# Performance work log

Measured on AMD Instinct MI355X. Metric: run time of the kernel, lower is better.

The kernel has to match this reference:

```python
import jax, jax.numpy as jnp
import numpy as np
from jax import lax

NUM_ITER = 10
SMOOTH = 1.0
CL_WEIGHT = 0.5


def _min_pool(x, wh, ww):
    # torch: -max_pool2d(-x) pads with -inf -> min-pool with +inf boundary
    return lax.reduce_window(x, jnp.inf, lax.min,
                             (1, 1, wh, ww), (1, 1, 1, 1),
                             [(0, 0), (0, 0), (wh // 2, wh // 2), (ww // 2, ww // 2)])


def _max_pool(x, wh, ww):
    return lax.reduce_window(x, -jnp.inf, lax.max,
                             (1, 1, wh, ww), (1, 1, 1, 1),
                             [(0, 0), (0, 0), (wh // 2, wh // 2), (ww // 2, ww // 2)])


def soft_erode(img):
    return jnp.minimum(_min_pool(img, 3, 1), _min_pool(img, 1, 3))


def soft_dilate(img):
    return _max_pool(img, 3, 3)


def soft_open(img):
    return soft_dilate(soft_erode(img))


def soft_skeleton(img, num_iter=NUM_ITER):
    # img: (B,1,H,W)
    skel = jax.nn.relu(img - soft_open(img))

    def body(i, carry):
        img_e, skel = carry
        img_e = soft_erode(img_e)
        delta = jax.nn.relu(img_e - soft_open(img_e))
        skel = skel + jax.nn.relu(delta - skel * delta)
        return (img_e, skel)

    _, skel = lax.fori_loop(0, num_iter, body, (img, skel))
    return skel


def soft_dice(pred, target, smooth=SMOOTH):
    inter = jnp.sum(pred * target)
    return (2.0 * inter + smooth) / (jnp.sum(pred) + jnp.sum(target) + smooth)


def setup_inputs() -> dict:
    key = jax.random.key(0)
    k1, k2 = jax.random.split(key)
    pred = jax.random.normal(k1, (8, 1, 1024, 1024), dtype=jnp.float32)
    target = jax.random.randint(k2, (8, 1, 1024, 1024), 0, 2, dtype=jnp.int32)
    return {"pred": pred, "target": target}


def reference(pred, target):
    pred_prob = jax.nn.sigmoid(pred)          # (B,1,H,W)
    target_f = target.astype(pred_prob.dtype)

    skel_pred = soft_skeleton(pred_prob)
    skel_target = soft_skeleton(target_f)

    tprec = (jnp.sum(skel_pred * target_f) + SMOOTH) / (jnp.sum(skel_pred) + SMOOTH)
    tsens = (jnp.sum(skel_target * pred_prob) + SMOOTH) / (jnp.sum(skel_target) + SMOOTH)
    cl_dice = 2.0 * tprec * tsens / (tprec + tsens + 1e-7)

    dice = soft_dice(pred_prob, target_f)
    combined = (1.0 - CL_WEIGHT) * dice + CL_WEIGHT * cl_dice
    loss = 1.0 - combined
    return loss
```

## Files before the change

kernel.cpp:

```cpp
#include <hip/hip_runtime.h>
#include <math.h>

#define IMG  1024
#define TILE 64
#define HALO 12
#define SPP  52
#define NPRED (90*SPP)
#define SEN2 0x40004000u

typedef _Float16 h2 __attribute__((ext_vector_type(2)));
union UH { unsigned u; h2 h; };
__device__ __forceinline__ h2 u2h(unsigned u){ UH x; x.u=u; return x.h; }
__device__ __forceinline__ unsigned h2u(h2 h){ UH x; x.h=h; return x.u; }
__device__ __forceinline__ h2 pmin(h2 a, h2 b){ return __builtin_elementwise_min(a,b); }
__device__ __forceinline__ h2 pmax(h2 a, h2 b){ return __builtin_elementwise_max(a,b); }
__device__ __forceinline__ h2 funnel(h2 hi_src, h2 lo_src){
  return u2h((h2u(lo_src)>>16) | (h2u(hi_src)<<16));
}
__device__ __forceinline__ unsigned dpp_shr1(unsigned old_, unsigned src){
  return (unsigned)__builtin_amdgcn_update_dpp((int)old_, (int)src, 0x111, 0xF, 0xF, false);
}
__device__ __forceinline__ unsigned dpp_shl1(unsigned old_, unsigned src){
  return (unsigned)__builtin_amdgcn_update_dpp((int)old_, (int)src, 0x101, 0xF, 0xF, false);
}
__device__ __forceinline__ float sigmoidf(float x){ return 1.0f/(1.0f+__expf(-x)); }
__device__ __forceinline__ h2 unsent(h2 x, h2 onev, h2 zerov){
  h2 t = pmax(x-onev, zerov); return x - t - t;
}
__device__ __forceinline__ unsigned extract8(unsigned w0, unsigned w1, unsigned w2, int bp){
  unsigned long long lo = (unsigned long long)w0 | ((unsigned long long)w1<<32);
  unsigned long long hi = (unsigned long long)w1 | ((unsigned long long)w2<<32);
  unsigned a = (unsigned)(lo >> bp);
  unsigned b = (unsigned)(hi >> (bp & 31));
  return ((bp < 32) ? a : b) & 0xFFu;
}
__device__ __forceinline__ uint4 erode5(uint4 rm, uint4 rc, uint4 rn, h2 lw, h2 rv){
  h2 a0=u2h(rc.x), a1=u2h(rc.y), a2=u2h(rc.z), a3=u2h(rc.w);
  h2 v0=pmin(u2h(rm.x), u2h(rn.x));
  h2 v1=pmin(u2h(rm.y), u2h(rn.y));
  h2 v2=pmin(u2h(rm.z), u2h(rn.z));
  h2 v3=pmin(u2h(rm.w), u2h(rn.w));
  h2 f0=funnel(a0,lw), f1=funnel(a1,a0), f2=funnel(a2,a1), f3=funnel(a3,a2), f4=funnel(rv,a3);
  uint4 e;
  e.x=h2u(pmin(pmin(f0,f1),pmin(v0,a0)));
  e.y=h2u(pmin(pmin(f1,f2),pmin(v1,a1)));
  e.z=h2u(pmin(pmin(f2,f3),pmin(v2,a2)));
  e.w=h2u(pmin(pmin(f3,f4),pmin(v3,a3)));
  return e;
}

template<bool BND>
__device__ void pipeline(const float* __restrict__ pred, const int* __restrict__ targ,
                         long base, int gr0, int gc0, int tid,
                         unsigned* A, unsigned* B, unsigned* Ta, unsigned* Tb,
                         h2 val[4], h2 skel[4], unsigned &tbits, unsigned &skbits) {
  for (int i = tid; i < 104; i += 512) {
    int r = (i < 52) ? 0 : 89, c = (i < 52) ? i : i - 52;
    A[r*SPP + c] = SEN2;  B[r*SPP + c] = SEN2;
  }
  for (int i = tid; i < 704; i += 512) {
    int r = 1 + (i >> 3), w = i & 7;
    w = (w < 2) ? w : 44 + w;
    A[r*SPP + w] = SEN2;  B[r*SPP + w] = SEN2;
  }
  if (!BND) {
    #pragma unroll
    for (int k=0;k<2;++k){
      int u = tid + (k<<9);
      if (u < 968){
        int r = u/11, q = u - r*11;
        long g = base + (long)(gr0+r)*IMG + gc0 + (q<<3);
        float4 pa = *(const float4*)(pred+g);
        float4 pb = *(const float4*)(pred+g+4);
        h2 w0 = {(_Float16)sigmoidf(pa.x), (_Float16)sigmoidf(pa.y)};
        h2 w1 = {(_Float16)sigmoidf(pa.z), (_Float16)sigmoidf(pa.w)};
        h2 w2 = {(_Float16)sigmoidf(pb.x), (_Float16)sigmoidf(pb.y)};
        h2 w3 = {(_Float16)sigmoidf(pb.z), (_Float16)sigmoidf(pb.w)};
        int o = (1+r)*SPP + 2 + (q<<2);
        uint2 d0; d0.x=h2u(w0); d0.y=h2u(w1);
        uint2 d1; d1.x=h2u(w2); d1.y=h2u(w3);
        *(uint2*)&A[o]   = d0;
        *(uint2*)&A[o+2] = d1;
      }
    }
    if (tid < 264){
      int u = tid;
      int r = u/3, w = u - r*3;
      long g = base + (long)(gr0+r)*IMG + gc0 + (w<<5);
      unsigned bits = 0;
      #pragma unroll
      for (int i=0;i<8;++i){
        if (w < 2 || i < 6) {
          int4 tv = *(const int4*)(targ + g + (i<<2));
          unsigned nib = (unsigned)(tv.x!=0) | ((unsigned)(tv.y!=0)<<1)
                       | ((unsigned)(tv.z!=0)<<2) | ((unsigned)(tv.w!=0)<<3);
          bits |= nib << (i<<2);
        }
      }
      if (w==2) bits |= 0xFF000000u;
      Ta[u] = bits;
    }
  } else {
    for (int i=tid; i<88*44; i+=512){
      int r = i/44, wd = i - r*44;
      int gr = gr0 + r;
      bool rok = (unsigned)gr < (unsigned)IMG;
      int gca = gc0 + (wd<<1), gcb = gca + 1;
      _Float16 va = (_Float16)2.0f, vb = (_Float16)2.0f;
      if (rok && (unsigned)gca < (unsigned)IMG) va = (_Float16)sigmoidf(pred[base + (long)gr*IMG + gca]);
      if (rok && (unsigned)gcb < (unsigned)IMG) vb = (_Float16)sigmoidf(pred[base + (long)gr*IMG + gcb]);
      h2 w; w.x = va; w.y = vb;
      A[(1+r)*SPP + 2 + wd] = h2u(w);
    }
    for (int u=tid; u<264; u+=512){
      int r = u/3, w = u - r*3;
      int gr = gr0 + r;
      bool rok = (unsigned)gr < (unsigned)IMG;
      unsigned bits = 0;
      for (int b=0;b<32;++b){
        int c = (w<<5) + b;
        unsigned bit = 1;
        if (c < 88) {
          int gc = gc0 + c;
          if (rok && (unsigned)gc < (unsigned)IMG) bit = (unsigned)(targ[base+(long)gr*IMG+gc] != 0);
        }
        bits |= bit << b;
      }
      Ta[u] = bits;
    }
  }
  __syncthreads();

  unsigned cm0=~0u, cm1=~0u, cm2=0x00FFFFFFu;
  bool colO = false;
  if (BND) {
    int lo = (-gc0 > 0) ? -gc0 : 0;
    int hi = (IMG - gc0 < 88) ? (IMG - gc0) : 88;
    colO = (lo > 0) || (hi < 88);
    unsigned m[3];
    #pragma unroll
    for (int w=0; w<3; ++w){
      int l = lo - (w<<5); if (l<0) l=0;
      int h = hi - (w<<5); if (h>32) h=32;
      unsigned mm = 0;
      if (h > l) {
        unsigned top = (h>=32)? ~0u : ((1u<<h)-1u);
        unsigned bot = (l<=0)? 0u : ((1u<<l)-1u);
        mm = top & ~bot;
      }
      m[w]=mm;
    }
    cm0=m[0]; cm1=m[1]; cm2=m[2] & 0x00FFFFFF;
  }

  const int es  = tid / 12,  eq  = tid - es*12;
  const int s2  = es*2;
  const int ew  = eq << 2;
  const bool has2 = (tid < 16);
  const int u2  = 512 + tid;
  const int es2 = u2/12, eq2 = u2 - es2*12;
  const int s2b = es2*2, ew2 = eq2<<2;

  const bool tex = (tid < 258);
  const int  to  = 3 + tid;
  const int  twd = tid % 3;

  const int qc = tid & 7;
  const int rg = tid >> 3;
  const int pr = HALO + rg;
  const int wq = 8 + (qc<<2);
  const int bp = 12 + (qc<<3);

  h2 ep[4];
  {
    uint4 a0 = *(const uint4*)&A[(pr+1)*SPP + wq];
    ep[0]=u2h(a0.x); ep[1]=u2h(a0.y); ep[2]=u2h(a0.z); ep[3]=u2h(a0.w);
    #pragma unroll
    for (int i=0;i<4;++i){ val[i]=ep[i]; skel[i]=(h2)(_Float16)0.0f; }
  }
  {
    int oa = pr*3;
    tbits = extract8(Ta[oa],Ta[oa+1],Ta[oa+2],bp);
  }
  unsigned tp0=0,tp1=0,tp2=0, sk0=0,sk1=0,sk2=0;
  const bool td = (tid < 64);
  const int tro = (12 + tid)*3;
  if (td) { tp0=Ta[tro]; tp1=Ta[tro+1]; tp2=Ta[tro+2]; }

  const h2 onev  = {(_Float16)1.0f,(_Float16)1.0f};
  const h2 zerov = {(_Float16)0.0f,(_Float16)0.0f};

  for (int j=0;j<11;++j){
    {
      auto ERO = [&](int s2_, int ew_, int eq_){
        uint4 rm = *(const uint4*)&A[s2_*SPP + ew_];
        uint4 rc = *(const uint4*)&A[(s2_+1)*SPP + ew_];
        #pragma unroll
        for (int t=0;t<2;++t){
          uint4 rn = *(const uint4*)&A[(s2_+2+t)*SPP + ew_];
          int brc = s2_+1+t;
          unsigned lwu = SEN2, rvu = SEN2;
          if (((tid&15)==0)  && (eq_!=0))  lwu = A[brc*SPP + ew_ - 1];
          if (((tid&15)==15) && (eq_!=11)) rvu = A[brc*SPP + ew_ + 4];
          lwu = dpp_shr1(lwu, rc.w);
          rvu = dpp_shl1(rvu, rc.x);
          if (eq_==0)  lwu = SEN2;
          if (eq_==11) rvu = SEN2;
          *(uint4*)&B[brc*SPP + ew_] = erode5(rm, rc, rn, u2h(lwu), u2h(rvu));
          rm = rc; rc = rn;
        }
      };
      if ((s2+1 >= j+1) && (s2 <= 86-j))
        ERO(s2, ew, eq);
      if (has2 && (s2b+1 >= j+1) && (s2b <= 86-j))
        ERO(s2b, ew2, eq2);
    }
    if (tex){
      unsigned own=Ta[to], up=Ta[to-3], dn=Ta[to+3];
      unsigned lef=0, rif=0;
      if (((tid&15)==0)  && (twd>0)) lef = Ta[to-1];
      if (((tid&15)==15) && (twd<2)) rif = Ta[to+1];
      unsigned le = dpp_shr1(lef, own);
      unsigned ri = dpp_shl1(rif, own);
      if (twd==0) le = ~0u;
      if (twd==2) ri = ~0u;
      unsigned h = own & ((own>>1)|(ri<<31)) & ((own<<1)|(le>>31));
      Tb[to] = h & up & dn;
    }
    __syncthreads();

    if (BND) {
      if (gr0 < 0) {
        for (int i=tid;i<12*44;i+=512){ int r=i/44; B[(1+r)*SPP+2+(i-r*44)] = SEN2; }
        if (tid < 36) Tb[tid] = ~0u;
      }
      if (gr0 + 88 > IMG) {
        for (int i=tid;i<12*44;i+=512){ int r=i/44; B[(77+r)*SPP+2+(i-r*44)] = SEN2; }
        if (tid < 36) Tb[228+tid] = ~0u;
      }
      if (colO) {
        if (gc0 < 0)
          for (int i=tid;i<88*6;i+=512){ int r=i/6; B[(1+r)*SPP+2+(i-r*6)] = SEN2; }
        if (gc0 + 88 > IMG)
          for (int i=tid;i<88*6;i+=512){ int r=i/6; B[(1+r)*SPP+40+(i-r*6)] = SEN2; }
        for (int i=tid;i<264;i+=512){
          int r=i/3, w=i-r*3;
          unsigned nm = (w==0)?~cm0:((w==1)?~cm1:~cm2);
          Tb[i] |= nm;
        }
      }
      __syncthreads();
    }

    {
      h2 vm[4];
      uint4 cap;
      #pragma unroll
      for (int k=0;k<3;++k){
        int ro = (pr+k)*SPP + wq;
        uint4 c = *(const uint4*)&B[ro];
        unsigned lwu = dpp_shr1(0u, c.w);
        unsigned rwu = dpp_shl1(0u, c.x);
        if (qc==0) lwu = B[ro-1];
        if (qc==7) rwu = B[ro+4];
        if (k==1) cap = c;
        h2 a0=u2h(c.x),a1=u2h(c.y),a2=u2h(c.z),a3=u2h(c.w);
        h2 lwv=u2h(lwu), rwv=u2h(rwu);
        if (BND){
          a0=unsent(a0,onev,zerov); a1=unsent(a1,onev,zerov);
          a2=unsent(a2,onev,zerov); a3=unsent(a3,onev,zerov);
          lwv=unsent(lwv,onev,zerov); rwv=unsent(rwv,onev,zerov);
        }
        h2 f0=funnel(a0,lwv), f1=funnel(a1,a0), f2=funnel(a2,a1), f3=funnel(a3,a2), f4=funnel(rwv,a3);
        h2 h0=pmax(pmax(f0,f1),a0);
        h2 h1=pmax(pmax(f1,f2),a1);
        h2 h2v=pmax(pmax(f2,f3),a2);
        h2 h3=pmax(pmax(f3,f4),a3);
        if (k==0){ vm[0]=h0; vm[1]=h1; vm[2]=h2v; vm[3]=h3; }
        else     { vm[0]=pmax(vm[0],h0); vm[1]=pmax(vm[1],h1);
                   vm[2]=pmax(vm[2],h2v); vm[3]=pmax(vm[3],h3); }
      }
      #pragma unroll
      for (int i=0;i<4;++i){
        h2 d0 = pmax(ep[i]-vm[i], zerov);
        h2 x0 = d0 - skel[i]*d0;
        skel[i] = skel[i] + pmax(x0, zerov);
      }
      ep[0]=u2h(cap.x); ep[1]=u2h(cap.y); ep[2]=u2h(cap.z); ep[3]=u2h(cap.w);
    }

    if (td) {
      unsigned o0=Tb[tro], o1=Tb[tro+1], o2=Tb[tro+2];
      unsigned u0=Tb[tro-3], u1=Tb[tro-2], u2v=Tb[tro-1];
      unsigned n0=Tb[tro+3], n1=Tb[tro+4], n2=Tb[tro+5];
      unsigned v0,v1,v2;
      if (BND){
        unsigned mu = ((unsigned)(gr0 + 11 + tid) < (unsigned)IMG) ? ~0u : 0u;
        unsigned md = ((unsigned)(gr0 + 13 + tid) < (unsigned)IMG) ? ~0u : 0u;
        v0 = ((u0&mu)|o0|(n0&md)) & cm0;
        v1 = ((u1&mu)|o1|(n1&md)) & cm1;
        v2 = ((u2v&mu)|o2|(n2&md)) & cm2;
      } else {
        v0 = u0|o0|n0; v1 = u1|o1|n1; v2 = u2v|o2|n2;
      }
      unsigned d0 = v0 | (v0<<1) | (v0>>1) | (v1<<31);
      unsigned d1 = v1 | (v1<<1) | (v0>>31) | (v1>>1) | (v2<<31);
      unsigned d2 = v2 | (v2<<1) | (v1>>31) | (v2>>1);
      sk0 |= tp0 & ~d0;
      sk1 |= tp1 & ~d1;
      sk2 |= tp2 & ~d2;
      tp0 = o0; tp1 = o1; tp2 = o2;
    }
    unsigned* t1 = A;  A = B;  B = t1;
    unsigned* t2 = Ta; Ta = Tb; Tb = t2;
  }

  __syncthreads();
  if (td){ Ta[3*tid]=sk0; Ta[3*tid+1]=sk1; Ta[3*tid+2]=sk2; }
  __syncthreads();
  {
    int o = rg*3;
    skbits = extract8(Ta[o],Ta[o+1],Ta[o+2],bp);
  }
}

__global__ __launch_bounds__(512,4)
void cl_dice_main(const float* __restrict__ pred, const int* __restrict__ targ,
                  float* __restrict__ ws) {
  __shared__ alignas(16) unsigned sPA[NPRED];
  __shared__ alignas(16) unsigned sPB[NPRED];
  __shared__ unsigned sTA[264], sTB[264];
  const int tid = threadIdx.x;
  const int gr0 = blockIdx.y * TILE - HALO;
  const int gc0 = blockIdx.x * TILE - HALO;
  const long base = (long)blockIdx.z * (long)(IMG * IMG);

  h2 val[4], skel[4]; unsigned tbits, skbits;
  const bool bnd = (blockIdx.x == 0) | (blockIdx.x == gridDim.x - 1) |
                   (blockIdx.y == 0) | (blockIdx.y == gridDim.y - 1);
  if (!bnd) pipeline<false>(pred, targ, base, gr0, gc0, tid, sPA, sPB, sTA, sTB, val, skel, tbits, skbits);
  else      pipeline<true >(pred, targ, base, gr0, gc0, tid, sPA, sPB, sTA, sTB, val, skel, tbits, skbits);

  float s[7] = {0,0,0,0,0,0,0};
  #pragma unroll
  for (int k=0;k<4;++k){
    int bb = k<<1;
    float p0=(float)val[k].x,  p1=(float)val[k].y;
    float a0=(float)skel[k].x, a1=(float)skel[k].y;
    float t0=(float)((tbits>>bb)&1u),  t1=(float)((tbits>>(bb+1))&1u);
    float b0=(float)((skbits>>bb)&1u), b1=(float)((skbits>>(bb+1))&1u);
    s[0]+=a0+a1;        s[1]+=a0*t0+a1*t1;
    s[2]+=b0+b1;        s[3]+=b0*p0+b1*p1;
    s[4]+=p0*t0+p1*t1;  s[5]+=p0+p1;  s[6]+=t0+t1;
  }

  float* red = (float*)sPA;
  #pragma unroll
  for (int k=0;k<7;++k){
    float v = s[k];
    v += __shfl_down(v,32); v += __shfl_down(v,16); v += __shfl_down(v,8);
    v += __shfl_down(v,4);  v += __shfl_down(v,2);  v += __shfl_down(v,1);
    if ((tid & 63) == 0) red[(tid>>6)*8 + k] = v;
  }
  __syncthreads();
  if (tid < 7) {
    float v = 0.f;
    #pragma unroll
    for (int w8=0; w8<8; ++w8) v += red[w8*8 + tid];
    int blk = (blockIdx.z * gridDim.y + blockIdx.y) * gridDim.x + blockIdx.x;
    ws[blk*8 + tid] = v;
  }
}

__global__ __launch_bounds__(256)
void cl_dice_finalize(const float* __restrict__ ws, float* __restrict__ out, int nblk) {
  __shared__ float red[4][8];
  int tid = threadIdx.x;
  float acc[7] = {0,0,0,0,0,0,0};
  for (int i=tid; i<nblk; i+=256) {
    #pragma unroll
    for (int k=0;k<7;++k) acc[k] += ws[i*8 + k];
  }
  #pragma unroll
  for (int k=0;k<7;++k){
    float v = acc[k];
    v += __shfl_down(v,32); v += __shfl_down(v,16); v += __shfl_down(v,8);
    v += __shfl_down(v,4);  v += __shfl_down(v,2);  v += __shfl_down(v,1);
    if ((tid & 63) == 0) red[tid>>6][k] = v;
  }
  __syncthreads();
  if (tid == 0) {
    float t0[7];
    #pragma unroll
    for (int k=0;k<7;++k) t0[k] = red[0][k] + red[1][k] + red[2][k] + red[3][k];
    float sum_sp = t0[0], sum_spt = t0[1], sum_st = t0[2], sum_stp = t0[3];
    float inter  = t0[4], sum_p   = t0[5], sum_t  = t0[6];
    float tprec = (sum_spt + 1.0f) / (sum_sp + 1.0f);
    float tsens = (sum_stp + 1.0f) / (sum_st + 1.0f);
    float cl    = 2.0f * tprec * tsens / (tprec + tsens + 1e-7f);
    float dice  = (2.0f * inter + 1.0f) / (sum_p + sum_t + 1.0f);
    out[0] = 1.0f - 0.5f * (dice + cl);
  }
}

extern "C" void kernel_launch(void* const* d_in, const int* in_sizes, int n_in,
                              void* d_out, int out_size, void* d_ws, size_t ws_size,
                              hipStream_t stream) {
  const float* pred = (const float*)d_in[0];
  const int*   targ = (const int*)d_in[1];
  float* ws  = (float*)d_ws;
  float* out = (float*)d_out;

  const int B = in_sizes[0] / (IMG * IMG);
  dim3 grid(IMG / TILE, IMG / TILE, B);
  cl_dice_main<<<grid, 512, 0, stream>>>(pred, targ, ws);

  const int nblk = (IMG / TILE) * (IMG / TILE) * B;
  cl_dice_finalize<<<1, 256, 0, stream>>>(ws, out, nblk);
}
```

Measured before the change: 240.7 us.

## Process two batch images per block to halve barrier count per image

```diff
diff --git a/kernel.cpp b/kernel.cpp
--- a/kernel.cpp
+++ b/kernel.cpp
@@ -49,19 +49,31 @@
   return e;
 }
 
+struct TS {
+  unsigned *A, *B, *Ta, *Tb;
+  h2 ep[4], val[4], skel[4];
+  unsigned tbits, skbits;
+  unsigned tp0,tp1,tp2, sk0,sk1,sk2;
+};
+
 template<bool BND>
-__device__ void pipeline(const float* __restrict__ pred, const int* __restrict__ targ,
-                         long base, int gr0, int gc0, int tid,
-                         unsigned* A, unsigned* B, unsigned* Ta, unsigned* Tb,
-                         h2 val[4], h2 skel[4], unsigned &tbits, unsigned &skbits) {
+__device__ void pipeline2(const float* __restrict__ pred, const int* __restrict__ targ,
+                          long baseX, long baseY, int gr0, int gc0, int tid,
+                          unsigned* sPA, unsigned* sPB, unsigned* sTA, unsigned* sTB,
+                          TS &X, TS &Y) {
+  X.A=sPA;       X.B=sPB;       X.Ta=sTA;     X.Tb=sTB;
+  Y.A=sPA+NPRED; Y.B=sPB+NPRED; Y.Ta=sTA+264; Y.Tb=sTB+264;
+
   for (int i = tid; i < 104; i += 512) {
     int r = (i < 52) ? 0 : 89, c = (i < 52) ? i : i - 52;
-    A[r*SPP + c] = SEN2;  B[r*SPP + c] = SEN2;
+    int o = r*SPP + c;
+    sPA[o]=SEN2; sPB[o]=SEN2; sPA[NPRED+o]=SEN2; sPB[NPRED+o]=SEN2;
   }
   for (int i = tid; i < 704; i += 512) {
     int r = 1 + (i >> 3), w = i & 7;
     w = (w < 2) ? w : 44 + w;
-    A[r*SPP + w] = SEN2;  B[r*SPP + w] = SEN2;
+    int o = r*SPP + w;
+    sPA[o]=SEN2; sPB[o]=SEN2; sPA[NPRED+o]=SEN2; sPB[NPRED+o]=SEN2;
   }
   if (!BND) {
     #pragma unroll
@@ -69,36 +81,54 @@
       int u = tid + (k<<9);
       if (u < 968){
         int r = u/11, q = u - r*11;
-        long g = base + (long)(gr0+r)*IMG + gc0 + (q<<3);
-        float4 pa = *(const float4*)(pred+g);
-        float4 pb = *(const float4*)(pred+g+4);
-        h2 w0 = {(_Float16)sigmoidf(pa.x), (_Float16)sigmoidf(pa.y)};
-        h2 w1 = {(_Float16)sigmoidf(pa.z), (_Float16)sigmoidf(pa.w)};
-        h2 w2 = {(_Float16)sigmoidf(pb.x), (_Float16)sigmoidf(pb.y)};
-        h2 w3 = {(_Float16)sigmoidf(pb.z), (_Float16)sigmoidf(pb.w)};
+        long go = (long)(gr0+r)*IMG + gc0 + (q<<3);
         int o = (1+r)*SPP + 2 + (q<<2);
-        uint2 d0; d0.x=h2u(w0); d0.y=h2u(w1);
-        uint2 d1; d1.x=h2u(w2); d1.y=h2u(w3);
-        *(uint2*)&A[o]   = d0;
-        *(uint2*)&A[o+2] = d1;
+        {
+          float4 pa = *(const float4*)(pred+baseX+go);
+          float4 pb = *(const float4*)(pred+baseX+go+4);
+          h2 w0 = {(_Float16)sigmoidf(pa.x), (_Float16)sigmoidf(pa.y)};
+          h2 w1 = {(_Float16)sigmoidf(pa.z), (_Float16)sigmoidf(pa.w)};
+          h2 w2 = {(_Float16)sigmoidf(pb.x), (_Float16)sigmoidf(pb.y)};
+          h2 w3 = {(_Float16)sigmoidf(pb.z), (_Float16)sigmoidf(pb.w)};
+          uint2 d0; d0.x=h2u(w0); d0.y=h2u(w1);
+          uint2 d1; d1.x=h2u(w2); d1.y=h2u(w3);
+          *(uint2*)&sPA[o]   = d0;
+          *(uint2*)&sPA[o+2] = d1;
+        }
+        {
+          float4 pa = *(const float4*)(pred+baseY+go);
+          float4 pb = *(const float4*)(pred+baseY+go+4);
+          h2 w0 = {(_Float16)sigmoidf(pa.x), (_Float16)sigmoidf(pa.y)};
+          h2 w1 = {(_Float16)sigmoidf(pa.z), (_Float16)sigmoidf(pa.w)};
+          h2 w2 = {(_Float16)sigmoidf(pb.x), (_Float16)sigmoidf(pb.y)};
+          h2 w3 = {(_Float16)sigmoidf(pb.z), (_Float16)sigmoidf(pb.w)};
+          uint2 d0; d0.x=h2u(w0); d0.y=h2u(w1);
+          uint2 d1; d1.x=h2u(w2); d1.y=h2u(w3);
+          *(uint2*)&sPA[NPRED+o]   = d0;
+          *(uint2*)&sPA[NPRED+o+2] = d1;
+        }
       }
     }
     if (tid < 264){
-      int u = tid;
-      int r = u/3, w = u - r*3;
-      long g = base + (long)(gr0+r)*IMG + gc0 + (w<<5);
-      unsigned bits = 0;
+      int r = tid/3, w = tid - r*3;
+      long go = (long)(gr0+r)*IMG + gc0 + (w<<5);
+      unsigned bitsX = 0, bitsY = 0;
       #pragma unroll
       for (int i=0;i<8;++i){
         if (w < 2 || i < 6) {
-          int4 tv = *(const int4*)(targ + g + (i<<2));
+          int4 tv = *(const int4*)(targ + baseX + go + (i<<2));
           unsigned nib = (unsigned)(tv.x!=0) | ((unsigned)(tv.y!=0)<<1)
                        | ((unsigned)(tv.z!=0)<<2) | ((unsigned)(tv.w!=0)<<3);
-          bits |= nib << (i<<2);
+          bitsX |= nib << (i<<2);
+          int4 tw = *(const int4*)(targ + baseY + go + (i<<2));
+          unsigned nib2 = (unsigned)(tw.x!=0) | ((unsigned)(tw.y!=0)<<1)
+                        | ((unsigned)(tw.z!=0)<<2) | ((unsigned)(tw.w!=0)<<3);
+          bitsY |= nib2 << (i<<2);
         }
       }
-      if (w==2) bits |= 0xFF000000u;
-      Ta[u] = bits;
+      if (w==2){ bitsX |= 0xFF000000u; bitsY |= 0xFF000000u; }
+      sTA[tid] = bitsX;
+      sTA[264+tid] = bitsY;
     }
   } else {
     for (int i=tid; i<88*44; i+=512){
@@ -106,27 +136,38 @@
       int gr = gr0 + r;
       bool rok = (unsigned)gr < (unsigned)IMG;
       int gca = gc0 + (wd<<1), gcb = gca + 1;
+      bool aok = rok && (unsigned)gca < (unsigned)IMG;
+      bool bok = rok && (unsigned)gcb < (unsigned)IMG;
+      long go = (long)gr*IMG;
       _Float16 va = (_Float16)2.0f, vb = (_Float16)2.0f;
-      if (rok && (unsigned)gca < (unsigned)IMG) va = (_Float16)sigmoidf(pred[base + (long)gr*IMG + gca]);
-      if (rok && (unsigned)gcb < (unsigned)IMG) vb = (_Float16)sigmoidf(pred[base + (long)gr*IMG + gcb]);
+      _Float16 ya = (_Float16)2.0f, yb = (_Float16)2.0f;
+      if (aok){ va = (_Float16)sigmoidf(pred[baseX + go + gca]);
+                ya = (_Float16)sigmoidf(pred[baseY + go + gca]); }
+      if (bok){ vb = (_Float16)sigmoidf(pred[baseX + go + gcb]);
+                yb = (_Float16)sigmoidf(pred[baseY + go + gcb]); }
       h2 w; w.x = va; w.y = vb;
-      A[(1+r)*SPP + 2 + wd] = h2u(w);
+      h2 y; y.x = ya; y.y = yb;
+      sPA[(1+r)*SPP + 2 + wd] = h2u(w);
+      sPA[NPRED + (1+r)*SPP + 2 + wd] = h2u(y);
     }
     for (int u=tid; u<264; u+=512){
       int r = u/3, w = u - r*3;
       int gr = gr0 + r;
       bool rok = (unsigned)gr < (unsigned)IMG;
-      unsigned bits = 0;
+      unsigned bitsX = 0, bitsY = 0;
       for (int b=0;b<32;++b){
         int c = (w<<5) + b;
-        unsigned bit = 1;
+        unsigned bx = 1, by = 1;
         if (c < 88) {
           int gc = gc0 + c;
-          if (rok && (unsigned)gc < (unsigned)IMG) bit = (unsigned)(targ[base+(long)gr*IMG+gc] != 0);
+          if (rok && (unsigned)gc < (unsigned)IMG){
+            bx = (unsigned)(targ[baseX+(long)gr*IMG+gc] != 0);
+            by = (unsigned)(targ[baseY+(long)gr*IMG+gc] != 0);
+          }
         }
-        bits |= bit << b;
-      }
-      Ta[u] = bits;
+        bitsX |= bx << b;  bitsY |= by << b;
+      }
+      sTA[u] = bitsX;  sTA[264+u] = bitsY;
     }
   }
   __syncthreads();
@@ -164,105 +205,100 @@
   const bool tex = (tid < 258);
   const int  to  = 3 + tid;
   const int  twd = tid % 3;
+  const bool flT = ((tid&15)==0)  && (twd>0);
+  const bool frT = ((tid&15)==15) && (twd<2);
 
   const int qc = tid & 7;
   const int rg = tid >> 3;
   const int pr = HALO + rg;
   const int wq = 8 + (qc<<2);
   const int bp = 12 + (qc<<3);
-
-  h2 ep[4];
-  {
-    uint4 a0 = *(const uint4*)&A[(pr+1)*SPP + wq];
-    ep[0]=u2h(a0.x); ep[1]=u2h(a0.y); ep[2]=u2h(a0.z); ep[3]=u2h(a0.w);
-    #pragma unroll
-    for (int i=0;i<4;++i){ val[i]=ep[i]; skel[i]=(h2)(_Float16)0.0f; }
-  }
-  {
-    int oa = pr*3;
-    tbits = extract8(Ta[oa],Ta[oa+1],Ta[oa+2],bp);
-  }
-  unsigned tp0=0,tp1=0,tp2=0, sk0=0,sk1=0,sk2=0;
+  const int tro = (12 + tid)*3;
   const bool td = (tid < 64);
-  const int tro = (12 + tid)*3;
-  if (td) { tp0=Ta[tro]; tp1=Ta[tro+1]; tp2=Ta[tro+2]; }
 
   const h2 onev  = {(_Float16)1.0f,(_Float16)1.0f};
   const h2 zerov = {(_Float16)0.0f,(_Float16)0.0f};
 
-  for (int j=0;j<11;++j){
-    {
-      auto ERO = [&](int s2_, int ew_, int eq_){
-        uint4 rm = *(const uint4*)&A[s2_*SPP + ew_];
-        uint4 rc = *(const uint4*)&A[(s2_+1)*SPP + ew_];
-        #pragma unroll
-        for (int t=0;t<2;++t){
-          uint4 rn = *(const uint4*)&A[(s2_+2+t)*SPP + ew_];
-          int brc = s2_+1+t;
-          unsigned lwu = SEN2, rvu = SEN2;
-          if (((tid&15)==0)  && (eq_!=0))  lwu = A[brc*SPP + ew_ - 1];
-          if (((tid&15)==15) && (eq_!=11)) rvu = A[brc*SPP + ew_ + 4];
-          lwu = dpp_shr1(lwu, rc.w);
-          rvu = dpp_shl1(rvu, rc.x);
-          if (eq_==0)  lwu = SEN2;
-          if (eq_==11) rvu = SEN2;
-          *(uint4*)&B[brc*SPP + ew_] = erode5(rm, rc, rn, u2h(lwu), u2h(rvu));
-          rm = rc; rc = rn;
-        }
-      };
-      if ((s2+1 >= j+1) && (s2 <= 86-j))
-        ERO(s2, ew, eq);
-      if (has2 && (s2b+1 >= j+1) && (s2b <= 86-j))
-        ERO(s2b, ew2, eq2);
-    }
+  auto INIT = [&](TS &t){
+    uint4 a0 = *(const uint4*)&t.A[(pr+1)*SPP + wq];
+    t.ep[0]=u2h(a0.x); t.ep[1]=u2h(a0.y); t.ep[2]=u2h(a0.z); t.ep[3]=u2h(a0.w);
+    #pragma unroll
+    for (int i=0;i<4;++i){ t.val[i]=t.ep[i]; t.skel[i]=(h2)(_Float16)0.0f; }
+    t.tbits = extract8(t.Ta[pr*3], t.Ta[pr*3+1], t.Ta[pr*3+2], bp);
+    t.tp0=0; t.tp1=0; t.tp2=0; t.sk0=0; t.sk1=0; t.sk2=0;
+    if (td){ t.tp0=t.Ta[tro]; t.tp1=t.Ta[tro+1]; t.tp2=t.Ta[tro+2]; }
+  };
+  INIT(X); INIT(Y);
+
+  auto ERODE = [&](TS &t, int j){
+    auto ero = [&](int s2_, int ew_, int eq_){
+      uint4 rm = *(const uint4*)&t.A[s2_*SPP + ew_];
+      uint4 rc = *(const uint4*)&t.A[(s2_+1)*SPP + ew_];
+      #pragma unroll
+      for (int tt=0;tt<2;++tt){
+        uint4 rn = *(const uint4*)&t.A[(s2_+2+tt)*SPP + ew_];
+        int brc = s2_+1+tt;
+        unsigned lwu = SEN2, rvu = SEN2;
+        if (((tid&15)==0)  && (eq_!=0))  lwu = t.A[brc*SPP + ew_ - 1];
+        if (((tid&15)==15) && (eq_!=11)) rvu = t.A[brc*SPP + ew_ + 4];
+        lwu = dpp_shr1(lwu, rc.w);
+        rvu = dpp_shl1(rvu, rc.x);
+        if (eq_==0)  lwu = SEN2;
+        if (eq_==11) rvu = SEN2;
+        *(uint4*)&t.B[brc*SPP + ew_] = erode5(rm, rc, rn, u2h(lwu), u2h(rvu));
+        rm = rc; rc = rn;
+      }
+    };
+    if ((s2+1 >= j+1) && (s2 <= 86-j))           ero(s2, ew, eq);
+    if (has2 && (s2b+1 >= j+1) && (s2b <= 86-j)) ero(s2b, ew2, eq2);
     if (tex){
-      unsigned own=Ta[to], up=Ta[to-3], dn=Ta[to+3];
+      unsigned own=t.Ta[to], up=t.Ta[to-3], dn=t.Ta[to+3];
       unsigned lef=0, rif=0;
-      if (((tid&15)==0)  && (twd>0)) lef = Ta[to-1];
-      if (((tid&15)==15) && (twd<2)) rif = Ta[to+1];
+      if (flT) lef = t.Ta[to-1];
+      if (frT) rif = t.Ta[to+1];
       unsigned le = dpp_shr1(lef, own);
       unsigned ri = dpp_shl1(rif, own);
       if (twd==0) le = ~0u;
       if (twd==2) ri = ~0u;
       unsigned h = own & ((own>>1)|(ri<<31)) & ((own<<1)|(le>>31));
-      Tb[to] = h & up & dn;
-    }
-    __syncthreads();
-
-    if (BND) {
-      if (gr0 < 0) {
-        for (int i=tid;i<12*44;i+=512){ int r=i/44; B[(1+r)*SPP+2+(i-r*44)] = SEN2; }
-        if (tid < 36) Tb[tid] = ~0u;
-      }
-      if (gr0 + 88 > IMG) {
-        for (int i=tid;i<12*44;i+=512){ int r=i/44; B[(77+r)*SPP+2+(i-r*44)] = SEN2; }
-        if (tid < 36) Tb[228+tid] = ~0u;
-      }
-      if (colO) {
-        if (gc0 < 0)
-          for (int i=tid;i<88*6;i+=512){ int r=i/6; B[(1+r)*SPP+2+(i-r*6)] = SEN2; }
-        if (gc0 + 88 > IMG)
-          for (int i=tid;i<88*6;i+=512){ int r=i/6; B[(1+r)*SPP+40+(i-r*6)] = SEN2; }
-        for (int i=tid;i<264;i+=512){
-          int r=i/3, w=i-r*3;
-          unsigned nm = (w==0)?~cm0:((w==1)?~cm1:~cm2);
-          Tb[i] |= nm;
-        }
-      }
-      __syncthreads();
-    }
-
+      t.Tb[to] = h & up & dn;
+    }
+  };
+
+  auto RESTAMP = [&](TS &t){
+    if (gr0 < 0) {
+      for (int i=tid;i<12*44;i+=512){ int r=i/44; t.B[(1+r)*SPP+2+(i-r*44)] = SEN2; }
+      if (tid < 36) t.Tb[tid] = ~0u;
+    }
+    if (gr0 + 88 > IMG) {
+      for (int i=tid;i<12*44;i+=512){ int r=i/44; t.B[(77+r)*SPP+2+(i-r*44)] = SEN2; }
+      if (tid < 36) t.Tb[228+tid] = ~0u;
+    }
+    if (colO) {
+      if (gc0 < 0)
+        for (int i=tid;i<88*6;i+=512){ int r=i/6; t.B[(1+r)*SPP+2+(i-r*6)] = SEN2; }
+      if (gc0 + 88 > IMG)
+        for (int i=tid;i<88*6;i+=512){ int r=i/6; t.B[(1+r)*SPP+40+(i-r*6)] = SEN2; }
+      for (int i=tid;i<264;i+=512){
+        int r=i/3, w=i-r*3;
+        unsigned nm = (w==0)?~cm0:((w==1)?~cm1:~cm2);
+        t.Tb[i] |= nm;
+      }
+    }
+  };
+
+  auto DILATE = [&](TS &t){
     {
       h2 vm[4];
       uint4 cap;
       #pragma unroll
       for (int k=0;k<3;++k){
         int ro = (pr+k)*SPP + wq;
-        uint4 c = *(const uint4*)&B[ro];
+        uint4 c = *(const uint4*)&t.B[ro];
         unsigned lwu = dpp_shr1(0u, c.w);
         unsigned rwu = dpp_shl1(0u, c.x);
-        if (qc==0) lwu = B[ro-1];
-        if (qc==7) rwu = B[ro+4];
+        if (qc==0) lwu = t.B[ro-1];
+        if (qc==7) rwu = t.B[ro+4];
         if (k==1) cap = c;
         h2 a0=u2h(c.x),a1=u2h(c.y),a2=u2h(c.z),a3=u2h(c.w);
         h2 lwv=u2h(lwu), rwv=u2h(rwu);
@@ -282,17 +318,16 @@
       }
       #pragma unroll
       for (int i=0;i<4;++i){
-        h2 d0 = pmax(ep[i]-vm[i], zerov);
-        h2 x0 = d0 - skel[i]*d0;
-        skel[i] = skel[i] + pmax(x0, zerov);
-      }
-      ep[0]=u2h(cap.x); ep[1]=u2h(cap.y); ep[2]=u2h(cap.z); ep[3]=u2h(cap.w);
-    }
-
+        h2 d0 = pmax(t.ep[i]-vm[i], zerov);
+        h2 x0 = d0 - t.skel[i]*d0;
+        t.skel[i] = t.skel[i] + pmax(x0, zerov);
+      }
+      t.ep[0]=u2h(cap.x); t.ep[1]=u2h(cap.y); t.ep[2]=u2h(cap.z); t.ep[3]=u2h(cap.w);
+    }
     if (td) {
-      unsigned o0=Tb[tro], o1=Tb[tro+1], o2=Tb[tro+2];
-      unsigned u0=Tb[tro-3], u1=Tb[tro-2], u2v=Tb[tro-1];
-      unsigned n0=Tb[tro+3], n1=Tb[tro+4], n2=Tb[tro+5];
+      unsigned o0=t.Tb[tro], o1=t.Tb[tro+1], o2=t.Tb[tro+2];
+      unsigned u0=t.Tb[tro-3], u1=t.Tb[tro-2], u2v=t.Tb[tro-1];
+      unsigned n0=t.Tb[tro+3], n1=t.Tb[tro+4], n2=t.Tb[tro+5];
       unsigned v0,v1,v2;
       if (BND){
         unsigned mu = ((unsigned)(gr0 + 11 + tid) < (unsigned)IMG) ? ~0u : 0u;
@@ -306,52 +341,74 @@
       unsigned d0 = v0 | (v0<<1) | (v0>>1) | (v1<<31);
       unsigned d1 = v1 | (v1<<1) | (v0>>31) | (v1>>1) | (v2<<31);
       unsigned d2 = v2 | (v2<<1) | (v1>>31) | (v2>>1);
-      sk0 |= tp0 & ~d0;
-      sk1 |= tp1 & ~d1;
-      sk2 |= tp2 & ~d2;
-      tp0 = o0; tp1 = o1; tp2 = o2;
-    }
-    unsigned* t1 = A;  A = B;  B = t1;
-    unsigned* t2 = Ta; Ta = Tb; Tb = t2;
+      t.sk0 |= t.tp0 & ~d0;
+      t.sk1 |= t.tp1 & ~d1;
+      t.sk2 |= t.tp2 & ~d2;
+      t.tp0 = o0; t.tp1 = o1; t.tp2 = o2;
+    }
+    unsigned* p1 = t.A;  t.A = t.B;  t.B = p1;
+    unsigned* p2 = t.Ta; t.Ta = t.Tb; t.Tb = p2;
+  };
+
+  for (int j=0;j<11;++j){
+    ERODE(X, j);
+    ERODE(Y, j);
+    __syncthreads();
+    if (BND) { RESTAMP(X); RESTAMP(Y); __syncthreads(); }
+    DILATE(X);
+    DILATE(Y);
   }
 
   __syncthreads();
-  if (td){ Ta[3*tid]=sk0; Ta[3*tid+1]=sk1; Ta[3*tid+2]=sk2; }
+  if (td){
+    X.Ta[3*tid]=X.sk0; X.Ta[3*tid+1]=X.sk1; X.Ta[3*tid+2]=X.sk2;
+    Y.Ta[3*tid]=Y.sk0; Y.Ta[3*tid+1]=Y.sk1; Y.Ta[3*tid+2]=Y.sk2;
+  }
   __syncthreads();
-  {
-    int o = rg*3;
-    skbits = extract8(Ta[o],Ta[o+1],Ta[o+2],bp);
-  }
-}
-
-__global__ __launch_bounds__(512,4)
+  X.skbits = extract8(X.Ta[rg*3], X.Ta[rg*3+1], X.Ta[rg*3+2], bp);
+  Y.skbits = extract8(Y.Ta[rg*3], Y.Ta[rg*3+1], Y.Ta[rg*3+2], bp);
+}
+
+__global__ __launch_bounds__(512,2)
 void cl_dice_main(const float* __restrict__ pred, const int* __restrict__ targ,
                   float* __restrict__ ws) {
-  __shared__ alignas(16) unsigned sPA[NPRED];
-  __shared__ alignas(16) unsigned sPB[NPRED];
-  __shared__ unsigned sTA[264], sTB[264];
+  __shared__ alignas(16) unsigned sPA[2*NPRED];
+  __shared__ alignas(16) unsigned sPB[2*NPRED];
+  __shared__ unsigned sTA[2*264], sTB[2*264];
   const int tid = threadIdx.x;
   const int gr0 = blockIdx.y * TILE - HALO;
   const int gc0 = blockIdx.x * TILE - HALO;
-  const long base = (long)blockIdx.z * (long)(IMG * IMG);
-
-  h2 val[4], skel[4]; unsigned tbits, skbits;
+  const long baseX = (long)blockIdx.z * (long)(IMG * IMG);
+  const long baseY = (long)(blockIdx.z + gridDim.z) * (long)(IMG * IMG);
+
+  TS X, Y;
   const bool bnd = (blockIdx.x == 0) | (blockIdx.x == gridDim.x - 1) |
                    (blockIdx.y == 0) | (blockIdx.y == gridDim.y - 1);
-  if (!bnd) pipeline<false>(pred, targ, base, gr0, gc0, tid, sPA, sPB, sTA, sTB, val, skel, tbits, skbits);
-  else      pipeline<true >(pred, targ, base, gr0, gc0, tid, sPA, sPB, sTA, sTB, val, skel, tbits, skbits);
+  if (!bnd) pipeline2<false>(pred, targ, baseX, baseY, gr0, gc0, tid, sPA, sPB, sTA, sTB, X, Y);
+  else      pipeline2<true >(pred, targ, baseX, baseY, gr0, gc0, tid, sPA, sPB, sTA, sTB, X, Y);
 
   float s[7] = {0,0,0,0,0,0,0};
   #pragma unroll
   for (int k=0;k<4;++k){
     int bb = k<<1;
-    float p0=(float)val[k].x,  p1=(float)val[k].y;
-    float a0=(float)skel[k].x, a1=(float)skel[k].y;
-    float t0=(float)((tbits>>bb)&1u),  t1=(float)((tbits>>(bb+1))&1u);
-    float b0=(float)((skbits>>bb)&1u), b1=(float)((skbits>>(bb+1))&1u);
-    s[0]+=a0+a1;        s[1]+=a0*t0+a1*t1;
-    s[2]+=b0+b1;        s[3]+=b0*p0+b1*p1;
-    s[4]+=p0*t0+p1*t1;  s[5]+=p0+p1;  s[6]+=t0+t1;
+    {
+      float p0=(float)X.val[k].x,  p1=(float)X.val[k].y;
+      float a0=(float)X.skel[k].x, a1=(float)X.skel[k].y;
+      float t0=(float)((X.tbits>>bb)&1u),  t1=(float)((X.tbits>>(bb+1))&1u);
+      float b0=(float)((X.skbits>>bb)&1u), b1=(float)((X.skbits>>(bb+1))&1u);
+      s[0]+=a0+a1;        s[1]+=a0*t0+a1*t1;
+      s[2]+=b0+b1;        s[3]+=b0*p0+b1*p1;
+      s[4]+=p0*t0+p1*t1;  s[5]+=p0+p1;  s[6]+=t0+t1;
+    }
+    {
+      float p0=(float)Y.val[k].x,  p1=(float)Y.val[k].y;
+      float a0=(float)Y.skel[k].x, a1=(float)Y.skel[k].y;
+      float t0=(float)((Y.tbits>>bb)&1u),  t1=(float)((Y.tbits>>(bb+1))&1u);
+      float b0=(float)((Y.skbits>>bb)&1u), b1=(float)((Y.skbits>>(bb+1))&1u);
+      s[0]+=a0+a1;        s[1]+=a0*t0+a1*t1;
+      s[2]+=b0+b1;        s[3]+=b0*p0+b1*p1;
+      s[4]+=p0*t0+p1*t1;  s[5]+=p0+p1;  s[6]+=t0+t1;
+    }
   }
 
   float* red = (float*)sPA;
@@ -412,9 +469,9 @@
   float* out = (float*)d_out;
 
   const int B = in_sizes[0] / (IMG * IMG);
-  dim3 grid(IMG / TILE, IMG / TILE, B);
+  dim3 grid(IMG / TILE, IMG / TILE, B/2);
   cl_dice_main<<<grid, 512, 0, stream>>>(pred, targ, ws);
 
-  const int nblk = (IMG / TILE) * (IMG / TILE) * B;
+  const int nblk = (IMG / TILE) * (IMG / TILE) * (B/2);
   cl_dice_finalize<<<1, 256, 0, stream>>>(ws, out, nblk);
 }
```

After: 259.6 us. +7.8%, slower.
